# Performance work log

Hardware: AMD Instinct MI355X
Metric: run time of the kernel (lower is better)

Reference implementation:

```python
import jax, jax.numpy as jnp
import numpy as np

B, S, D, H = 1, 2048, 4096, 32
HD = D // H  # 128


def _rope_params(seq_len, head_dim, base=10000.0):
    inv_freq = 1.0 / (base ** (np.arange(0, head_dim, 2, dtype=np.float64) / head_dim))
    ang = np.outer(np.arange(seq_len, dtype=np.float64), inv_freq)      # [S, HD/2]
    ang = np.concatenate([ang, ang], axis=-1)                            # [S, HD]
    return jnp.asarray(np.cos(ang), jnp.float32), jnp.asarray(np.sin(ang), jnp.float32)


def _apply_rope(x, cos, sin):
    # x: [B, H, S, HD]; cos/sin: [S, HD]
    half = x.shape[-1] // 2
    x1, x2 = x[..., :half], x[..., half:]
    rotated = jnp.concatenate([-x2, x1], axis=-1)
    return x * cos[None, None] + rotated * sin[None, None]


def setup_inputs() -> dict:
    key = jax.random.key(0)
    ks = jax.random.split(key, 6)
    w_scale = 1.0 / np.sqrt(D)
    X = jax.random.normal(ks[0], (B, S, D), jnp.float32)
    Wq = jax.random.normal(ks[1], (D, D), jnp.float32) * w_scale
    Wk = jax.random.normal(ks[2], (D, D), jnp.float32) * w_scale
    Wv = jax.random.normal(ks[3], (D, D), jnp.float32) * w_scale
    Wo = jax.random.normal(ks[4], (D, D), jnp.float32) * w_scale
    bo = jax.random.normal(ks[5], (D,), jnp.float32) * 0.01
    cos, sin = _rope_params(S, HD)
    return {"X": X, "Wq": Wq, "Wk": Wk, "Wv": Wv, "Wo": Wo, "bo": bo, "cos": cos, "sin": sin}


def reference(X, Wq, Wk, Wv, Wo, bo, cos, sin):
    b, s, d = X.shape
    # nn.Linear: y = x @ W.T
    def split_heads(y):
        return y.reshape(b, s, H, HD).transpose(0, 2, 1, 3)  # [B,H,S,HD]
    q = split_heads(X @ Wq.T)
    k = split_heads(X @ Wk.T)
    v = split_heads(X @ Wv.T)
    q = _apply_rope(q, cos, sin)
    k = _apply_rope(k, cos, sin)
    scores = jnp.einsum('bhqd,bhkd->bhqk', q, k) / np.sqrt(HD).astype(np.float32)
    causal = jnp.tril(jnp.ones((s, s), bool))
    scores = jnp.where(causal[None, None], scores, -jnp.inf)
    attn = jax.nn.softmax(scores, axis=-1)
    out = jnp.einsum('bhqk,bhkd->bhqd', attn, v)  # [B,H,S,HD]
    out = out.transpose(0, 2, 1, 3).reshape(b, s, d)
    return out @ Wo.T + bo
```

## Files before the change

### kernel.cpp

```cpp
#include <hip/hip_runtime.h>

typedef unsigned short u16;
typedef __attribute__((ext_vector_type(8))) short s16x8;
typedef __attribute__((ext_vector_type(4))) float f32x4;

__device__ __forceinline__ u16 f2bf(float f) {
  unsigned u = __float_as_uint(f);
  u += 0x7fffu + ((u >> 16) & 1u);
  return (u16)(u >> 16);
}
__device__ __forceinline__ float bf2f(u16 h) {
  return __uint_as_float(((unsigned)h) << 16);
}

typedef __attribute__((address_space(1))) const void gvoid_t;
typedef __attribute__((address_space(3))) void lvoid_t;
__device__ __forceinline__ void gload_lds16(const void* g, void* l) {
  __builtin_amdgcn_global_load_lds((gvoid_t*)g, (lvoid_t*)l, 16, 0, 0);
}

__global__ void cvt_f32_bf16(const float* __restrict__ in, u16* __restrict__ out, int n) {
  int i = (blockIdx.x * 256 + threadIdx.x) * 4;
  if (i >= n) return;
  float4 v = *(const float4*)(in + i);
  ushort4 o;
  o.x = f2bf(v.x); o.y = f2bf(v.y); o.z = f2bf(v.z); o.w = f2bf(v.w);
  *(ushort4*)(out + i) = o;
}

template<typename OutT, bool BIAS>
__global__ __launch_bounds__(512) void gemm_bt2(
    const u16* __restrict__ A, const u16* __restrict__ Bm,
    OutT* __restrict__ C, const float* __restrict__ bias,
    int M, int N, int K)
{
  __shared__ u16 As[3][128 * 64];
  __shared__ u16 Bs[3][256 * 64];

  const int t = threadIdx.x;
  const int lane = t & 63, wid = t >> 6;
  const int wm = wid >> 2, wn = wid & 3;
  const int lr = lane & 15, lk = lane >> 4;

  const int wg = blockIdx.x;
  const int xcd = wg & 7, j = wg >> 3;
  const int m0 = (j & 15) * 128;
  const int n0 = ((xcd << 1) | (j >> 4)) * 256;

  const int nt = K >> 6;

  f32x4 acc[4][4] = {};

#define STAGE(KT)                                                              \
  {                                                                            \
    const int bu_ = ((unsigned)(KT)) % 3u;                                     \
    const int k0_ = (KT) << 6;                                                 \
    _Pragma("unroll")                                                          \
    for (int it = 0; it < 2; ++it) {                                           \
      int id = it * 512 + t;                                                   \
      int r = id >> 3, c0 = id & 7;                                            \
      gload_lds16(A + (size_t)(m0 + r) * K + k0_ + ((c0 ^ (r & 7)) << 3),      \
                  &As[bu_][id * 8]);                                           \
    }                                                                          \
    _Pragma("unroll")                                                          \
    for (int it = 0; it < 4; ++it) {                                           \
      int id = it * 512 + t;                                                   \
      int r = id >> 3, c0 = id & 7;                                            \
      gload_lds16(Bm + (size_t)(n0 + r) * K + k0_ + ((c0 ^ (r & 7)) << 3),     \
                  &Bs[bu_][id * 8]);                                           \
    }                                                                          \
  }

  STAGE(0);
  STAGE(1);
  asm volatile("s_waitcnt vmcnt(6)" ::: "memory");
  __builtin_amdgcn_s_barrier();
  __builtin_amdgcn_sched_barrier(0);

  for (int kt = 0; kt < nt; ++kt) {
    const int bu = ((unsigned)kt) % 3u;
    if (kt + 2 < nt) STAGE(kt + 2);

    __builtin_amdgcn_s_setprio(1);
#pragma unroll
    for (int ks = 0; ks < 2; ++ks) {
      s16x8 af[4], bf[4];
#pragma unroll
      for (int i = 0; i < 4; ++i) {
        int ra = wm * 64 + i * 16 + lr;
        af[i] = *(const s16x8*)&As[bu][ra * 64 + (((ks * 4 + lk) ^ (ra & 7)) << 3)];
        int rb = wn * 64 + i * 16 + lr;
        bf[i] = *(const s16x8*)&Bs[bu][rb * 64 + (((ks * 4 + lk) ^ (rb & 7)) << 3)];
      }
#pragma unroll
      for (int i = 0; i < 4; ++i)
#pragma unroll
        for (int jn = 0; jn < 4; ++jn)
          acc[i][jn] = __builtin_amdgcn_mfma_f32_16x16x32_bf16(af[i], bf[jn], acc[i][jn], 0, 0, 0);
    }
    __builtin_amdgcn_s_setprio(0);

    asm volatile("s_waitcnt lgkmcnt(0)" ::: "memory");
    if (kt + 2 < nt)       { asm volatile("s_waitcnt vmcnt(6)" ::: "memory"); }
    else if (kt + 2 == nt) { asm volatile("s_waitcnt vmcnt(0)" ::: "memory"); }
    if (kt + 1 < nt) {
      __builtin_amdgcn_s_barrier();
      __builtin_amdgcn_sched_barrier(0);
    }
  }
#undef STAGE

#pragma unroll
  for (int i = 0; i < 4; ++i) {
    int row_b = m0 + wm * 64 + i * 16 + lk * 4;
#pragma unroll
    for (int jn = 0; jn < 4; ++jn) {
      int col = n0 + wn * 64 + jn * 16 + lr;
      float bv = BIAS ? bias[col] : 0.f;
#pragma unroll
      for (int r = 0; r < 4; ++r) {
        float v = acc[i][jn][r] + bv;
        size_t off = (size_t)(row_b + r) * N + col;
        if constexpr (sizeof(OutT) == 2) ((u16*)C)[off] = f2bf(v);
        else                             ((float*)C)[off] = v;
      }
    }
  }
}

__global__ void rope_qk(u16* __restrict__ Q, u16* __restrict__ Kt,
                        const float* __restrict__ cosp, const float* __restrict__ sinp) {
  int i = blockIdx.x * 256 + threadIdx.x;
  int d = i & 63;
  int h = (i >> 6) & 31;
  int s = i >> 11;
  float c = cosp[s * 128 + d], sn = sinp[s * 128 + d];
  size_t base = (size_t)s * 4096 + h * 128 + d;
  float q1 = bf2f(Q[base]), q2 = bf2f(Q[base + 64]);
  Q[base]      = f2bf(q1 * c - q2 * sn);
  Q[base + 64] = f2bf(q2 * c + q1 * sn);
  float k1 = bf2f(Kt[base]), k2 = bf2f(Kt[base + 64]);
  Kt[base]      = f2bf(k1 * c - k2 * sn);
  Kt[base + 64] = f2bf(k2 * c + k1 * sn);
}

__global__ __launch_bounds__(512) void flash_attn(
    const u16* __restrict__ Q, const u16* __restrict__ Kg, const u16* __restrict__ Vg,
    u16* __restrict__ Ctx)
{
  const int D = 4096;
  __shared__ u16 Ks[2][64 * 128];
  __shared__ u16 Vt[2][128 * 64];
  __shared__ u16 Ps[8][16 * 64];

  const int t = threadIdx.x, lane = t & 63, wid = t >> 6;
  const int lr = lane & 15, lk = lane >> 4;

  const int wg = blockIdx.x;
  const int xcd = wg & 7, j = wg >> 3;
  const int bx = 15 - (j >> 2);
  const int h = xcd * 4 + (j & 3);
  const int q0 = bx * 128;
  const int qw0 = q0 + wid * 16;

  s16x8 qf[4];
#pragma unroll
  for (int kc = 0; kc < 4; ++kc)
    qf[kc] = *(const s16x8*)(Q + (size_t)(qw0 + lr) * D + h * 128 + kc * 32 + lk * 8);

  f32x4 o[8] = {};
  float m_r[4] = {-1e30f, -1e30f, -1e30f, -1e30f};
  float l_r[4] = {0.f, 0.f, 0.f, 0.f};

  const int ntiles = 2 * bx + 2;
  const float scale2 = 0.12751779f;

  const int ch = t & 15, kv2 = (t >> 4) * 2;

  {
    const u16* src = Vg + (size_t)kv2 * D + h * 128 + ch * 8;
    s16x8 a0 = *(const s16x8*)src;
    s16x8 a1 = *(const s16x8*)(src + D);
#pragma unroll
    for (int it = 0; it < 2; ++it) {
      int id = it * 512 + t;
      int kv = id >> 4, c0 = id & 15;
      gload_lds16(Kg + (size_t)kv * D + h * 128 + ((c0 ^ (kv & 7)) << 3), &Ks[0][id * 8]);
    }
#pragma unroll
    for (int jj = 0; jj < 8; ++jj) {
      int d = ch * 8 + jj;
      int sw = ((ch ^ jj) & 7) << 3;
      unsigned pr = (unsigned)(u16)a0[jj] | ((unsigned)(u16)a1[jj] << 16);
      *(unsigned*)&Vt[0][d * 64 + (kv2 ^ sw)] = pr;
    }
  }

  for (int kt = 0; kt < ntiles; ++kt) {
    const int b = kt & 1;
    const int kv0 = kt * 64;
    __syncthreads();

    s16x8 a0, a1;
    const bool pf = (kt + 1 < ntiles);
    if (pf) {
      const u16* src = Vg + (size_t)(kv0 + 64 + kv2) * D + h * 128 + ch * 8;
      a0 = *(const s16x8*)src;
      a1 = *(const s16x8*)(src + D);
#pragma unroll
      for (int it = 0; it < 2; ++it) {
        int id = it * 512 + t;
        int kv = id >> 4, c0 = id & 15;
        gload_lds16(Kg + (size_t)(kv0 + 64 + kv) * D + h * 128 + ((c0 ^ (kv & 7)) << 3),
                    &Ks[b ^ 1][id * 8]);
      }
    }

    if (kv0 <= qw0 + 15) {
      const bool masked = (kv0 + 63 > qw0);

      f32x4 st[4] = {};
      __builtin_amdgcn_s_setprio(1);
#pragma unroll
      for (int nt = 0; nt < 4; ++nt) {
        int kv = nt * 16 + lr;
        int sw = kv & 7;
#pragma unroll
        for (int kc = 0; kc < 4; ++kc) {
          s16x8 kf = *(const s16x8*)&Ks[b][kv * 128 + (((4 * kc + lk) ^ sw) << 3)];
          st[nt] = __builtin_amdgcn_mfma_f32_16x16x32_bf16(qf[kc], kf, st[nt], 0, 0, 0);
        }
      }
      __builtin_amdgcn_s_setprio(0);

      float pmax_[4];
#pragma unroll
      for (int r = 0; r < 4; ++r) {
        int q_r = qw0 + lk * 4 + r;
        if (masked) {
#pragma unroll
          for (int nt = 0; nt < 4; ++nt) {
            float sv = st[nt][r] * scale2;
            if (kv0 + nt * 16 + lr > q_r) sv = -1e30f;
            st[nt][r] = sv;
          }
        } else {
#pragma unroll
          for (int nt = 0; nt < 4; ++nt) st[nt][r] *= scale2;
        }
        float pm = fmaxf(fmaxf(st[0][r], st[1][r]), fmaxf(st[2][r], st[3][r]));
        pm = fmaxf(pm, __shfl_xor(pm, 1));
        pm = fmaxf(pm, __shfl_xor(pm, 2));
        pm = fmaxf(pm, __shfl_xor(pm, 4));
        pm = fmaxf(pm, __shfl_xor(pm, 8));
        pmax_[r] = pm;
      }
      bool nr = (pmax_[0] > m_r[0] + 8.f) || (pmax_[1] > m_r[1] + 8.f) ||
                (pmax_[2] > m_r[2] + 8.f) || (pmax_[3] > m_r[3] + 8.f);
      if (__any(nr)) {
#pragma unroll
        for (int r = 0; r < 4; ++r) {
          float mn = fmaxf(m_r[r], pmax_[r]);
          float al = __builtin_amdgcn_exp2f(m_r[r] - mn);
          m_r[r] = mn; l_r[r] *= al;
#pragma unroll
          for (int nb = 0; nb < 8; ++nb) o[nb][r] *= al;
        }
      }
#pragma unroll
      for (int r = 0; r < 4; ++r) {
        int ql = lk * 4 + r;
        int swp = ((ql >> 1) & 7) << 3;
        float ps = 0.f;
#pragma unroll
        for (int nt = 0; nt < 4; ++nt) {
          float pv = __builtin_amdgcn_exp2f(st[nt][r] - m_r[r]);
          ps += pv;
          Ps[wid][ql * 64 + ((nt * 16 + lr) ^ swp)] = f2bf(pv);
        }
        ps += __shfl_xor(ps, 1);
        ps += __shfl_xor(ps, 2);
        ps += __shfl_xor(ps, 4);
        ps += __shfl_xor(ps, 8);
        l_r[r] += ps;
      }
      asm volatile("s_waitcnt lgkmcnt(0)" ::: "memory");

      s16x8 pa[2];
#pragma unroll
      for (int ks = 0; ks < 2; ++ks) {
        int col = (ks * 32 + lk * 8) ^ (((lr >> 1) & 7) << 3);
        pa[ks] = *(const s16x8*)&Ps[wid][lr * 64 + col];
      }

      __builtin_amdgcn_s_setprio(1);
#pragma unroll
      for (int ks = 0; ks < 2; ++ks) {
#pragma unroll
        for (int nb = 0; nb < 8; ++nb) {
          int d = nb * 16 + lr;
          int g = (((d >> 3) ^ d) & 7) << 3;
          s16x8 vf = *(const s16x8*)&Vt[b][d * 64 + ((ks * 32 + lk * 8) ^ g)];
          o[nb] = __builtin_amdgcn_mfma_f32_16x16x32_bf16(pa[ks], vf, o[nb], 0, 0, 0);
        }
      }
      __builtin_amdgcn_s_setprio(0);
    }

    if (pf) {
#pragma unroll
      for (int jj = 0; jj < 8; ++jj) {
        int d = ch * 8 + jj;
        int sw = ((ch ^ jj) & 7) << 3;
        unsigned pr = (unsigned)(u16)a0[jj] | ((unsigned)(u16)a1[jj] << 16);
        *(unsigned*)&Vt[b ^ 1][d * 64 + (kv2 ^ sw)] = pr;
      }
    }
  }

#pragma unroll
  for (int r = 0; r < 4; ++r) {
    float inv = 1.f / l_r[r];
    int q_r = qw0 + lk * 4 + r;
#pragma unroll
    for (int nb = 0; nb < 8; ++nb)
      Ctx[(size_t)q_r * D + h * 128 + nb * 16 + lr] = f2bf(o[nb][r] * inv);
  }
}

extern "C" void kernel_launch(void* const* d_in, const int* in_sizes, int n_in,
                              void* d_out, int out_size, void* d_ws, size_t ws_size,
                              hipStream_t stream) {
  const int S = 2048, D = 4096, H = 32;
  const size_t SD = (size_t)S * D, DD = (size_t)D * D;

  const float* X  = (const float*)d_in[0];
  const float* Wq = (const float*)d_in[1];
  const float* Wk = (const float*)d_in[2];
  const float* Wv = (const float*)d_in[3];
  const float* Wo = (const float*)d_in[4];
  const float* bo = (const float*)d_in[5];
  const float* cs = (const float*)d_in[6];
  const float* sn = (const float*)d_in[7];

  u16* WB = (u16*)d_ws;
  u16* Xb = WB + DD;
  u16* Qb = Xb + SD;
  u16* Kb = Qb + SD;
  u16* Vb = Kb + SD;

  dim3 blk(256);
  dim3 g2(256);
  dim3 b2(512);

  cvt_f32_bf16<<<(int)(SD / 1024), blk, 0, stream>>>(X, Xb, (int)SD);
  cvt_f32_bf16<<<(int)(DD / 1024), blk, 0, stream>>>(Wq, WB, (int)DD);
  gemm_bt2<u16, false><<<g2, b2, 0, stream>>>(Xb, WB, Qb, nullptr, S, D, D);
  cvt_f32_bf16<<<(int)(DD / 1024), blk, 0, stream>>>(Wk, WB, (int)DD);
  gemm_bt2<u16, false><<<g2, b2, 0, stream>>>(Xb, WB, Kb, nullptr, S, D, D);
  cvt_f32_bf16<<<(int)(DD / 1024), blk, 0, stream>>>(Wv, WB, (int)DD);
  gemm_bt2<u16, false><<<g2, b2, 0, stream>>>(Xb, WB, Vb, nullptr, S, D, D);

  rope_qk<<<(S * H * 64) / 256, blk, 0, stream>>>(Qb, Kb, cs, sn);

  flash_attn<<<dim3(512), dim3(512), 0, stream>>>(Qb, Kb, Vb, Xb );

  cvt_f32_bf16<<<(int)(DD / 1024), blk, 0, stream>>>(Wo, WB, (int)DD);
  gemm_bt2<float, true><<<g2, b2, 0, stream>>>(Xb, WB, (float*)d_out, bo, S, D, D);
}
```

Baseline: 576.6 us.

## Interleave GEMM global prefetch with split MFMA phases using ping-pong barriers

Restructures the GEMM main loop so each k-substep is split into two MFMA halves over A rows. The prefetch loads for tile kt+2 are spread across these phases, and barriers are added between phases so waves interleave LDS reads, global loads and MFMA work. The aim is to hide global-to-LDS load issue and LDS read latency behind matrix-core work. In exchange there are many more barriers per iteration, and the vmcnt accounting must stay correct since the load order changed.

```diff
diff --git a/kernel.cpp b/kernel.cpp
--- a/kernel.cpp
+++ b/kernel.cpp
@@ -51,7 +51,7 @@
 
   f32x4 acc[4][4] = {};
 
-#define STAGE(KT)                                                              \
+#define STAGE_A(KT)                                                            \
   {                                                                            \
     const int bu_ = ((unsigned)(KT)) % 3u;                                     \
     const int k0_ = (KT) << 6;                                                 \
@@ -62,53 +62,82 @@
       gload_lds16(A + (size_t)(m0 + r) * K + k0_ + ((c0 ^ (r & 7)) << 3),      \
                   &As[bu_][id * 8]);                                           \
     }                                                                          \
+  }
+#define STAGE_B(KT, HALF)                                                      \
+  {                                                                            \
+    const int bu_ = ((unsigned)(KT)) % 3u;                                     \
+    const int k0_ = (KT) << 6;                                                 \
     _Pragma("unroll")                                                          \
-    for (int it = 0; it < 4; ++it) {                                           \
-      int id = it * 512 + t;                                                   \
+    for (int it = 0; it < 2; ++it) {                                           \
+      int id = ((HALF) * 2 + it) * 512 + t;                                    \
       int r = id >> 3, c0 = id & 7;                                            \
       gload_lds16(Bm + (size_t)(n0 + r) * K + k0_ + ((c0 ^ (r & 7)) << 3),     \
                   &Bs[bu_][id * 8]);                                           \
     }                                                                          \
   }
 
-  STAGE(0);
-  STAGE(1);
+  STAGE_A(0); STAGE_B(0, 0); STAGE_B(0, 1);
+  STAGE_A(1); STAGE_B(1, 0); STAGE_B(1, 1);
   asm volatile("s_waitcnt vmcnt(6)" ::: "memory");
   __builtin_amdgcn_s_barrier();
-  __builtin_amdgcn_sched_barrier(0);
 
   for (int kt = 0; kt < nt; ++kt) {
     const int bu = ((unsigned)kt) % 3u;
-    if (kt + 2 < nt) STAGE(kt + 2);
-
-    __builtin_amdgcn_s_setprio(1);
+    const bool st = (kt + 2 < nt);
+
 #pragma unroll
     for (int ks = 0; ks < 2; ++ks) {
-      s16x8 af[4], bf[4];
-#pragma unroll
-      for (int i = 0; i < 4; ++i) {
-        int ra = wm * 64 + i * 16 + lr;
-        af[i] = *(const s16x8*)&As[bu][ra * 64 + (((ks * 4 + lk) ^ (ra & 7)) << 3)];
-        int rb = wn * 64 + i * 16 + lr;
-        bf[i] = *(const s16x8*)&Bs[bu][rb * 64 + (((ks * 4 + lk) ^ (rb & 7)) << 3)];
-      }
-#pragma unroll
-      for (int i = 0; i < 4; ++i)
+      s16x8 bf[4];
+#pragma unroll
+      for (int jn = 0; jn < 4; ++jn) {
+        int rb = wn * 64 + jn * 16 + lr;
+        bf[jn] = *(const s16x8*)&Bs[bu][rb * 64 + (((ks * 4 + lk) ^ (rb & 7)) << 3)];
+      }
+      s16x8 af0[2];
+#pragma unroll
+      for (int ii = 0; ii < 2; ++ii) {
+        int ra = wm * 64 + ii * 16 + lr;
+        af0[ii] = *(const s16x8*)&As[bu][ra * 64 + (((ks * 4 + lk) ^ (ra & 7)) << 3)];
+      }
+      if (st) { if (ks == 0) STAGE_A(kt + 2) else STAGE_B(kt + 2, 1) }
+      __builtin_amdgcn_s_barrier();
+      asm volatile("s_waitcnt lgkmcnt(0)" ::: "memory");
+      __builtin_amdgcn_sched_barrier(0);
+      __builtin_amdgcn_s_setprio(1);
+#pragma unroll
+      for (int ii = 0; ii < 2; ++ii)
 #pragma unroll
         for (int jn = 0; jn < 4; ++jn)
-          acc[i][jn] = __builtin_amdgcn_mfma_f32_16x16x32_bf16(af[i], bf[jn], acc[i][jn], 0, 0, 0);
-    }
-    __builtin_amdgcn_s_setprio(0);
-
-    asm volatile("s_waitcnt lgkmcnt(0)" ::: "memory");
-    if (kt + 2 < nt)       { asm volatile("s_waitcnt vmcnt(6)" ::: "memory"); }
-    else if (kt + 2 == nt) { asm volatile("s_waitcnt vmcnt(0)" ::: "memory"); }
-    if (kt + 1 < nt) {
+          acc[ii][jn] = __builtin_amdgcn_mfma_f32_16x16x32_bf16(af0[ii], bf[jn], acc[ii][jn], 0, 0, 0);
+      __builtin_amdgcn_s_setprio(0);
       __builtin_amdgcn_s_barrier();
+
+      s16x8 af1[2];
+#pragma unroll
+      for (int ii = 0; ii < 2; ++ii) {
+        int ra = wm * 64 + (2 + ii) * 16 + lr;
+        af1[ii] = *(const s16x8*)&As[bu][ra * 64 + (((ks * 4 + lk) ^ (ra & 7)) << 3)];
+      }
+      if (st && ks == 0) STAGE_B(kt + 2, 0);
+      if (ks == 1) {
+        if (st)                { asm volatile("s_waitcnt vmcnt(6)" ::: "memory"); }
+        else if (kt + 2 == nt) { asm volatile("s_waitcnt vmcnt(0)" ::: "memory"); }
+      }
+      __builtin_amdgcn_s_barrier();
+      asm volatile("s_waitcnt lgkmcnt(0)" ::: "memory");
       __builtin_amdgcn_sched_barrier(0);
-    }
-  }
-#undef STAGE
+      __builtin_amdgcn_s_setprio(1);
+#pragma unroll
+      for (int ii = 0; ii < 2; ++ii)
+#pragma unroll
+        for (int jn = 0; jn < 4; ++jn)
+          acc[2 + ii][jn] = __builtin_amdgcn_mfma_f32_16x16x32_bf16(af1[ii], bf[jn], acc[2 + ii][jn], 0, 0, 0);
+      __builtin_amdgcn_s_setprio(0);
+      if (!(ks == 1 && kt == nt - 1)) __builtin_amdgcn_s_barrier();
+    }
+  }
+#undef STAGE_A
+#undef STAGE_B
 
 #pragma unroll
   for (int i = 0; i < 4; ++i) {
```

After: 618.6 us. +7.3%, slower.
